# Kernel tuning notes

Measured on AMD Instinct MI355X. Metric: run time of the kernel, lower is better.

The kernel has to match this reference:

```python
import jax, jax.numpy as jnp
import numpy as np

N_HEADS = 4
SIGMA = 6.0
T_IN = 12
T_TOTAL = 24


def setup_inputs() -> dict:
    key = jax.random.key(0)
    k1, k2, k3, k4, k5 = jax.random.split(key, 5)
    B, T, N, C, K = 16, T_IN, 5000, 4, 16
    x = jax.random.normal(k1, (B, T, N, C), dtype=jnp.float32)
    dists = jax.random.uniform(k2, (N, K), dtype=jnp.float32) * 10.0  # kNN distances
    neighbors = jax.random.randint(k3, (N, K), 0, N)                  # kNN indices
    d_in = T * N_HEADS                   # 48
    d_out = T_TOTAL - T_IN               # 12
    W = jax.random.normal(k4, (d_in, d_out), dtype=jnp.float32) * (1.0 / np.sqrt(d_in))
    b = jax.random.normal(k5, (d_out,), dtype=jnp.float32) * 0.01
    return {"x": x, "dists": dists, "W": W, "b": b, "neighbors": neighbors}


def reference(x, dists, W, b, neighbors):
    B, T, N, C = x.shape
    H = N_HEADS
    # lambda_h = h/H for h = 1..H
    lam = jnp.arange(1, H + 1, dtype=x.dtype) / H                     # [H]
    # weights[n,k,h] = exp(-d_{nk}^2 * lam_h / sigma^2)
    w = jnp.exp(-(dists ** 2)[:, :, None] * lam / (SIGMA ** 2))       # [N,K,H]
    # gather neighbor features: [B,T,N,K,C]
    xg = x[:, :, neighbors, :]
    # distance-weighted aggregation over neighbors -> [B,T,N,H,C]
    agg = jnp.einsum('btnkc,nkh->btnhc', xg, w)
    # permute (0,2,4,1,3) -> [B,N,C,T,H], flatten last two -> [B,N,C,T*H]
    feat = jnp.transpose(agg, (0, 2, 4, 1, 3)).reshape(B, N, C, T * H)
    # shrink: Linear + ReLU -> [B,N,C,T_TOTAL-T]
    y = jax.nn.relu(feat @ W + b)
    # -> [B, T_TOTAL-T, N, C]
    y = jnp.transpose(y, (0, 3, 1, 2))
    return jnp.concatenate([x, y], axis=1)                            # [B,T_TOTAL,N,C]
```

## Files before the change

### kernel.cpp

```cpp
#include <hip/hip_runtime.h>

#define Bz 16
#define Tin 12
#define Ttot 24
#define NN 5000
#define KK 16
#define HH 4
#define OO 12
#define TH 48
#define G  8
#define JJ 24

typedef float nfloat4 __attribute__((ext_vector_type(4)));
typedef float f2 __attribute__((ext_vector_type(2)));

__device__ __forceinline__ float4 nt_load4(const float4* p) {
    nfloat4 v = __builtin_nontemporal_load((const nfloat4*)p);
    return *(float4*)&v;
}
__device__ __forceinline__ void nt_store4(float4 v, float4* p) {
    __builtin_nontemporal_store(*(nfloat4*)&v, (nfloat4*)p);
}

#define K1_NB 64
#define K1_BT 24
#define K1_TILES 79

__global__ __launch_bounds__(256) void transpose_concat_kernel(
    const float4* __restrict__ x4,
    float4* __restrict__ xT2,
    float4* __restrict__ out4)
{
    __shared__ float4 tile[K1_BT][K1_NB + 1];
    const int bid = blockIdx.x;
    const int g   = bid & 7;
    const int n0  = (bid >> 3) * K1_NB;
    const int bt0 = g * K1_BT;
    const int rem = min(K1_NB, NN - n0);
    const int tid = threadIdx.x;

    #pragma unroll
    for (int r = 0; r < (K1_NB * K1_BT) / 256; r++) {
        int tau = r * 256 + tid;
        int j = tau / K1_NB;
        int i = tau % K1_NB;
        if (i < rem) {
            int bt = bt0 + j;
            float4 v = nt_load4(&x4[(size_t)bt * NN + n0 + i]);
            tile[j][i] = v;
            int b = bt / Tin, t = bt - b * Tin;
            nt_store4(v, &out4[(size_t)(b * Ttot + t) * NN + n0 + i]);
        }
    }
    __syncthreads();

    #pragma unroll
    for (int r = 0; r < (K1_NB * K1_BT) / 256; r++) {
        int tau = r * 256 + tid;
        int i = tau / K1_BT;
        int j = tau - i * K1_BT;
        if (i < rem) {
            xT2[((size_t)g * NN + (n0 + i)) * JJ + j] = tile[j][i];
        }
    }
}

#define NPB 8
#define FSB2 49
#define FSN2 99
#define WTS  52

__global__ __launch_bounds__(192) void gnn_main_kernel(
    const float4* __restrict__ xT2,
    const float* __restrict__ dists,
    const float* __restrict__ W,
    const float* __restrict__ bias,
    const int*   __restrict__ nbrs,
    float4* __restrict__ out4)
{
    __shared__ float4 feat[NPB * FSN2];
    __shared__ float4 w4_s[NPB][KK + 1];
    __shared__ float  Wt_s[OO * WTS];
    __shared__ float  bias_s[OO];
    __shared__ int    nbroff_s[NPB][KK + 1];

    const int bid = blockIdx.x;
    const int g   = bid & 7;
    const int n0  = (bid >> 3) * NPB;
    const int tid = threadIdx.x;

    for (int i = tid; i < OO * WTS; i += 192) {
        int o = i / WTS, col = i - o * WTS;
        if (col < TH) Wt_s[i] = W[col * OO + o];
    }
    if (tid < OO) bias_s[tid] = bias[tid];
    if (tid < NPB * KK) {
        int nl = tid >> 4, k = tid & 15;
        nbroff_s[nl][k] = nbrs[(n0 + nl) * KK + k] * (JJ * (int)sizeof(float4));
        float d = dists[(n0 + nl) * KK + k];
        float p = expf(-(d * d) * (1.0f / 144.0f));
        float4 wv;
        wv.x = p;
        wv.y = p * p;
        wv.z = wv.y * p;
        wv.w = wv.y * wv.y;
        w4_s[nl][k] = wv;
    }
    __syncthreads();

    {
        const int nl  = tid / JJ;
        const int j   = tid - nl * JJ;
        const int b_l = j / Tin;
        const int t   = j - b_l * Tin;
        const char* xgb = (const char*)xT2 + (size_t)g * (NN * JJ * sizeof(float4));
        const unsigned j16 = (unsigned)j * 16u;

        f2 a0l = {0,0}, a0h = {0,0}, a1l = {0,0}, a1h = {0,0};
        f2 a2l = {0,0}, a2h = {0,0}, a3l = {0,0}, a3h = {0,0};
        #pragma unroll
        for (int k = 0; k < KK; k++) {
            unsigned off = (unsigned)nbroff_s[nl][k] + j16;
            float4 xv = *(const float4*)(xgb + off);
            f2 xl = {xv.x, xv.y}, xh = {xv.z, xv.w};
            float4 wv = w4_s[nl][k];
            f2 w0 = {wv.x, wv.x}, w1 = {wv.y, wv.y};
            f2 w2 = {wv.z, wv.z}, w3 = {wv.w, wv.w};
            a0l += w0 * xl; a0h += w0 * xh;
            a1l += w1 * xl; a1h += w1 * xh;
            a2l += w2 * xl; a2h += w2 * xh;
            a3l += w3 * xl; a3h += w3 * xh;
        }
        const int base = nl * FSN2 + b_l * FSB2 + t;
        feat[base +  0] = float4{a0l.x, a0l.y, a0h.x, a0h.y};
        feat[base + 12] = float4{a1l.x, a1l.y, a1h.x, a1h.y};
        feat[base + 24] = float4{a2l.x, a2l.y, a2h.x, a2h.y};
        feat[base + 36] = float4{a3l.x, a3l.y, a3h.x, a3h.y};
    }
    __syncthreads();

    if (tid < 64) {
        const int nl   = tid & 7;
        const int rest = tid >> 3;
        const int b_l  = rest & 1;
        const int o3   = rest >> 1;
        const int o0   = 3 * o3;

        float4 acc[3];
        #pragma unroll
        for (int i = 0; i < 3; i++) {
            float bz = bias_s[o0 + i];
            acc[i] = float4{bz, bz, bz, bz};
        }
        const int fb = nl * FSN2 + b_l * FSB2;
        #pragma unroll
        for (int t = 0; t < Tin; t++) {
            float4 f0 = feat[fb + t];
            float4 f1 = feat[fb + 12 + t];
            float4 fq = feat[fb + 24 + t];
            float4 f3 = feat[fb + 36 + t];
            f2 f0l = {f0.x, f0.y}, f0h = {f0.z, f0.w};
            f2 f1l = {f1.x, f1.y}, f1h = {f1.z, f1.w};
            f2 f2l = {fq.x, fq.y}, f2h = {fq.z, fq.w};
            f2 f3l = {f3.x, f3.y}, f3h = {f3.z, f3.w};
            #pragma unroll
            for (int i = 0; i < 3; i++) {
                const float4 wq = *(const float4*)&Wt_s[(o0 + i) * WTS + t * 4];
                f2 al = {acc[i].x, acc[i].y}, ah = {acc[i].z, acc[i].w};
                f2 wx = {wq.x, wq.x}, wy = {wq.y, wq.y};
                f2 wz = {wq.z, wq.z}, ww = {wq.w, wq.w};
                al += wx * f0l; ah += wx * f0h;
                al += wy * f1l; ah += wy * f1h;
                al += wz * f2l; ah += wz * f2h;
                al += ww * f3l; ah += ww * f3h;
                acc[i] = float4{al.x, al.y, ah.x, ah.y};
            }
        }
        const int b = g * 2 + b_l;
        #pragma unroll
        for (int i = 0; i < 3; i++) {
            int o = o0 + i;
            float4 y = acc[i];
            y.x = fmaxf(y.x, 0.0f); y.y = fmaxf(y.y, 0.0f);
            y.z = fmaxf(y.z, 0.0f); y.w = fmaxf(y.w, 0.0f);
            nt_store4(y, &out4[(size_t)(b * Ttot + Tin + o) * NN + n0 + nl]);
        }
    }
}

extern "C" void kernel_launch(void* const* d_in, const int* in_sizes, int n_in,
                              void* d_out, int out_size, void* d_ws, size_t ws_size,
                              hipStream_t stream) {
    const float* x     = (const float*)d_in[0];
    const float* dists = (const float*)d_in[1];
    const float* W     = (const float*)d_in[2];
    const float* bias  = (const float*)d_in[3];
    const int*   nbrs  = (const int*)d_in[4];
    float4* out4 = (float4*)d_out;
    float4* xT2  = (float4*)d_ws;

    hipLaunchKernelGGL(transpose_concat_kernel, dim3(K1_TILES * G), dim3(256), 0,
                       stream, (const float4*)x, xT2, out4);

    hipLaunchKernelGGL(gnn_main_kernel, dim3((NN / NPB) * G), dim3(192), 0, stream,
                       (const float4*)xT2, dists, W, bias, nbrs, out4);
}
```

Baseline: 109.0 us.

## Assign gather work per XCC via atomic counters and loop multiple node chunks per block

The main kernel now reads its XCC id from a hardware register and claims work from a per-XCC atomic counter. Each XCC then processes one batch group g, so that group's transposed slice of x stays in that XCC's L2. When an XCC's counter is exhausted, the block steals from other XCCs with CAS. Each block now handles 5 consecutive 8-node chunks, which cuts the grid from 5000 blocks to 1000 and amortizes the W/bias shared-memory setup. The costs are atomics, an extra sync per chunk, reliance on an undocumented hardware register read, and less parallelism per launch.

```diff
diff --git a/kernel.cpp b/kernel.cpp
--- a/kernel.cpp
+++ b/kernel.cpp
@@ -29,7 +29,8 @@
 __global__ __launch_bounds__(256) void transpose_concat_kernel(
     const float4* __restrict__ x4,
     float4* __restrict__ xT2,
-    float4* __restrict__ out4)
+    float4* __restrict__ out4,
+    int* __restrict__ k2ctr)
 {
     __shared__ float4 tile[K1_BT][K1_NB + 1];
     const int bid = blockIdx.x;
@@ -38,6 +39,8 @@
     const int bt0 = g * K1_BT;
     const int rem = min(K1_NB, NN - n0);
     const int tid = threadIdx.x;
+
+    if (bid == 0 && tid < G) k2ctr[tid] = 0;
 
     #pragma unroll
     for (int r = 0; r < (K1_NB * K1_BT) / 256; r++) {
@@ -66,6 +69,8 @@
 }
 
 #define NPB 8
+#define CPB 5
+#define CAP 125
 #define FSB2 49
 #define FSN2 99
 #define WTS  52
@@ -76,115 +81,144 @@
     const float* __restrict__ W,
     const float* __restrict__ bias,
     const int*   __restrict__ nbrs,
-    float4* __restrict__ out4)
+    float4* __restrict__ out4,
+    int* __restrict__ ctr)
 {
     __shared__ float4 feat[NPB * FSN2];
     __shared__ float4 w4_s[NPB][KK + 1];
     __shared__ float  Wt_s[OO * WTS];
     __shared__ float  bias_s[OO];
     __shared__ int    nbroff_s[NPB][KK + 1];
-
-    const int bid = blockIdx.x;
-    const int g   = bid & 7;
-    const int n0  = (bid >> 3) * NPB;
+    __shared__ int    work_s;
+
     const int tid = threadIdx.x;
+
+    int xcc;
+    asm volatile("s_getreg_b32 %0, hwreg(HW_REG_XCC_ID)" : "=s"(xcc));
+    xcc &= 7;
+
+    if (tid == 0) {
+        int gg  = xcc;
+        int idx = atomicAdd(&ctr[gg], 1);
+        if (idx >= CAP) {
+            idx = -1;
+            for (int a = 1; a < 8 && idx < 0; a++) {
+                int g2  = (xcc + a) & 7;
+                int old = atomicAdd(&ctr[g2], 0);
+                while (old < CAP) {
+                    int prev = atomicCAS(&ctr[g2], old, old + 1);
+                    if (prev == old) { idx = old; gg = g2; break; }
+                    old = prev;
+                }
+            }
+            if (idx < 0) idx = 0;
+        }
+        work_s = gg * CAP + idx;
+    }
 
     for (int i = tid; i < OO * WTS; i += 192) {
         int o = i / WTS, col = i - o * WTS;
         if (col < TH) Wt_s[i] = W[col * OO + o];
     }
     if (tid < OO) bias_s[tid] = bias[tid];
-    if (tid < NPB * KK) {
-        int nl = tid >> 4, k = tid & 15;
-        nbroff_s[nl][k] = nbrs[(n0 + nl) * KK + k] * (JJ * (int)sizeof(float4));
-        float d = dists[(n0 + nl) * KK + k];
-        float p = expf(-(d * d) * (1.0f / 144.0f));
-        float4 wv;
-        wv.x = p;
-        wv.y = p * p;
-        wv.z = wv.y * p;
-        wv.w = wv.y * wv.y;
-        w4_s[nl][k] = wv;
-    }
     __syncthreads();
 
-    {
-        const int nl  = tid / JJ;
-        const int j   = tid - nl * JJ;
-        const int b_l = j / Tin;
-        const int t   = j - b_l * Tin;
-        const char* xgb = (const char*)xT2 + (size_t)g * (NN * JJ * sizeof(float4));
-        const unsigned j16 = (unsigned)j * 16u;
-
-        f2 a0l = {0,0}, a0h = {0,0}, a1l = {0,0}, a1h = {0,0};
-        f2 a2l = {0,0}, a2h = {0,0}, a3l = {0,0}, a3h = {0,0};
-        #pragma unroll
-        for (int k = 0; k < KK; k++) {
-            unsigned off = (unsigned)nbroff_s[nl][k] + j16;
-            float4 xv = *(const float4*)(xgb + off);
-            f2 xl = {xv.x, xv.y}, xh = {xv.z, xv.w};
-            float4 wv = w4_s[nl][k];
-            f2 w0 = {wv.x, wv.x}, w1 = {wv.y, wv.y};
-            f2 w2 = {wv.z, wv.z}, w3 = {wv.w, wv.w};
-            a0l += w0 * xl; a0h += w0 * xh;
-            a1l += w1 * xl; a1h += w1 * xh;
-            a2l += w2 * xl; a2h += w2 * xh;
-            a3l += w3 * xl; a3h += w3 * xh;
-        }
-        const int base = nl * FSN2 + b_l * FSB2 + t;
-        feat[base +  0] = float4{a0l.x, a0l.y, a0h.x, a0h.y};
-        feat[base + 12] = float4{a1l.x, a1l.y, a1h.x, a1h.y};
-        feat[base + 24] = float4{a2l.x, a2l.y, a2h.x, a2h.y};
-        feat[base + 36] = float4{a3l.x, a3l.y, a3h.x, a3h.y};
-    }
-    __syncthreads();
-
-    if (tid < 64) {
-        const int nl   = tid & 7;
-        const int rest = tid >> 3;
-        const int b_l  = rest & 1;
-        const int o3   = rest >> 1;
-        const int o0   = 3 * o3;
-
-        float4 acc[3];
-        #pragma unroll
-        for (int i = 0; i < 3; i++) {
-            float bz = bias_s[o0 + i];
-            acc[i] = float4{bz, bz, bz, bz};
-        }
-        const int fb = nl * FSN2 + b_l * FSB2;
-        #pragma unroll
-        for (int t = 0; t < Tin; t++) {
-            float4 f0 = feat[fb + t];
-            float4 f1 = feat[fb + 12 + t];
-            float4 fq = feat[fb + 24 + t];
-            float4 f3 = feat[fb + 36 + t];
-            f2 f0l = {f0.x, f0.y}, f0h = {f0.z, f0.w};
-            f2 f1l = {f1.x, f1.y}, f1h = {f1.z, f1.w};
-            f2 f2l = {fq.x, fq.y}, f2h = {fq.z, fq.w};
-            f2 f3l = {f3.x, f3.y}, f3h = {f3.z, f3.w};
+    const int g      = work_s / CAP;
+    const int chunk5 = work_s - g * CAP;
+    const char* xgb  = (const char*)xT2 + (size_t)g * (NN * JJ * sizeof(float4));
+
+    for (int q = 0; q < CPB; q++) {
+        const int n0 = (chunk5 * CPB + q) * NPB;
+
+        if (tid < NPB * KK) {
+            int nl = tid >> 4, k = tid & 15;
+            nbroff_s[nl][k] = nbrs[(n0 + nl) * KK + k] * (JJ * (int)sizeof(float4));
+            float d = dists[(n0 + nl) * KK + k];
+            float p = expf(-(d * d) * (1.0f / 144.0f));
+            float4 wv;
+            wv.x = p; wv.y = p * p; wv.z = wv.y * p; wv.w = wv.y * wv.y;
+            w4_s[nl][k] = wv;
+        }
+        __syncthreads();
+
+        {
+            const int nl  = tid / JJ;
+            const int j   = tid - nl * JJ;
+            const int b_l = j / Tin;
+            const int t   = j - b_l * Tin;
+            const unsigned j16 = (unsigned)j * 16u;
+
+            f2 a0l = {0,0}, a0h = {0,0}, a1l = {0,0}, a1h = {0,0};
+            f2 a2l = {0,0}, a2h = {0,0}, a3l = {0,0}, a3h = {0,0};
+            #pragma unroll
+            for (int k = 0; k < KK; k++) {
+                unsigned off = (unsigned)nbroff_s[nl][k] + j16;
+                float4 xv = *(const float4*)(xgb + off);
+                f2 xl = {xv.x, xv.y}, xh = {xv.z, xv.w};
+                float4 wv = w4_s[nl][k];
+                f2 w0 = {wv.x, wv.x}, w1 = {wv.y, wv.y};
+                f2 w2 = {wv.z, wv.z}, w3 = {wv.w, wv.w};
+                a0l += w0 * xl; a0h += w0 * xh;
+                a1l += w1 * xl; a1h += w1 * xh;
+                a2l += w2 * xl; a2h += w2 * xh;
+                a3l += w3 * xl; a3h += w3 * xh;
+            }
+            const int base = nl * FSN2 + b_l * FSB2 + t;
+            feat[base +  0] = float4{a0l.x, a0l.y, a0h.x, a0h.y};
+            feat[base + 12] = float4{a1l.x, a1l.y, a1h.x, a1h.y};
+            feat[base + 24] = float4{a2l.x, a2l.y, a2h.x, a2h.y};
+            feat[base + 36] = float4{a3l.x, a3l.y, a3h.x, a3h.y};
+        }
+        __syncthreads();
+
+        if (tid < 64) {
+            const int nl   = tid & 7;
+            const int rest = tid >> 3;
+            const int b_l  = rest & 1;
+            const int o3   = rest >> 1;
+            const int o0   = 3 * o3;
+
+            float4 acc[3];
             #pragma unroll
             for (int i = 0; i < 3; i++) {
-                const float4 wq = *(const float4*)&Wt_s[(o0 + i) * WTS + t * 4];
-                f2 al = {acc[i].x, acc[i].y}, ah = {acc[i].z, acc[i].w};
-                f2 wx = {wq.x, wq.x}, wy = {wq.y, wq.y};
-                f2 wz = {wq.z, wq.z}, ww = {wq.w, wq.w};
-                al += wx * f0l; ah += wx * f0h;
-                al += wy * f1l; ah += wy * f1h;
-                al += wz * f2l; ah += wz * f2h;
-                al += ww * f3l; ah += ww * f3h;
-                acc[i] = float4{al.x, al.y, ah.x, ah.y};
-            }
-        }
-        const int b = g * 2 + b_l;
-        #pragma unroll
-        for (int i = 0; i < 3; i++) {
-            int o = o0 + i;
-            float4 y = acc[i];
-            y.x = fmaxf(y.x, 0.0f); y.y = fmaxf(y.y, 0.0f);
-            y.z = fmaxf(y.z, 0.0f); y.w = fmaxf(y.w, 0.0f);
-            nt_store4(y, &out4[(size_t)(b * Ttot + Tin + o) * NN + n0 + nl]);
-        }
+                float bz = bias_s[o0 + i];
+                acc[i] = float4{bz, bz, bz, bz};
+            }
+            const int fb = nl * FSN2 + b_l * FSB2;
+            #pragma unroll
+            for (int t = 0; t < Tin; t++) {
+                float4 f0 = feat[fb + t];
+                float4 f1 = feat[fb + 12 + t];
+                float4 fq = feat[fb + 24 + t];
+                float4 f3 = feat[fb + 36 + t];
+                f2 f0l = {f0.x, f0.y}, f0h = {f0.z, f0.w};
+                f2 f1l = {f1.x, f1.y}, f1h = {f1.z, f1.w};
+                f2 f2l = {fq.x, fq.y}, f2h = {fq.z, fq.w};
+                f2 f3l = {f3.x, f3.y}, f3h = {f3.z, f3.w};
+                #pragma unroll
+                for (int i = 0; i < 3; i++) {
+                    const float4 wq = *(const float4*)&Wt_s[(o0 + i) * WTS + t * 4];
+                    f2 al = {acc[i].x, acc[i].y}, ah = {acc[i].z, acc[i].w};
+                    f2 wx = {wq.x, wq.x}, wy = {wq.y, wq.y};
+                    f2 wz = {wq.z, wq.z}, ww = {wq.w, wq.w};
+                    al += wx * f0l; ah += wx * f0h;
+                    al += wy * f1l; ah += wy * f1h;
+                    al += wz * f2l; ah += wz * f2h;
+                    al += ww * f3l; ah += ww * f3h;
+                    acc[i] = float4{al.x, al.y, ah.x, ah.y};
+                }
+            }
+            const int b = g * 2 + b_l;
+            #pragma unroll
+            for (int i = 0; i < 3; i++) {
+                int o = o0 + i;
+                float4 y = acc[i];
+                y.x = fmaxf(y.x, 0.0f); y.y = fmaxf(y.y, 0.0f);
+                y.z = fmaxf(y.z, 0.0f); y.w = fmaxf(y.w, 0.0f);
+                nt_store4(y, &out4[(size_t)(b * Ttot + Tin + o) * NN + n0 + nl]);
+            }
+        }
+        __syncthreads();
     }
 }
 
@@ -198,10 +232,11 @@
     const int*   nbrs  = (const int*)d_in[4];
     float4* out4 = (float4*)d_out;
     float4* xT2  = (float4*)d_ws;
+    int*    ctr  = (int*)((char*)d_ws + 15360000);
 
     hipLaunchKernelGGL(transpose_concat_kernel, dim3(K1_TILES * G), dim3(256), 0,
-                       stream, (const float4*)x, xT2, out4);
-
-    hipLaunchKernelGGL(gnn_main_kernel, dim3((NN / NPB) * G), dim3(192), 0, stream,
-                       (const float4*)xT2, dists, W, bias, nbrs, out4);
-}
+                       stream, (const float4*)x, xT2, out4, ctr);
+
+    hipLaunchKernelGGL(gnn_main_kernel, dim3(G * CAP), dim3(192), 0, stream,
+                       (const float4*)xT2, dists, W, bias, nbrs, out4, ctr);
+}
```

Measured after the change: 127.0 us. 16.5% more time.
